# Kernel tuning notes

Hardware: AMD Instinct MI355X
Metric: run time of the kernel (lower is better)

The kernel has to match this reference:

```python
import jax, jax.numpy as jnp
import numpy as np

N = 8192      # number of graph nodes
C = 256       # feature_size
D = C // 2    # projection dim


def setup_inputs() -> dict:
    key = jax.random.key(0)
    ks = jax.random.split(key, 10)
    s_in = 1.0 / np.sqrt(C + 3)   # torch Linear default init scale (uniform bound)
    s_r = 1.0 / np.sqrt(D)
    return {
        "landmarks": jax.random.normal(ks[0], (1, N, 3), dtype=jnp.float32),
        "features": jax.random.normal(ks[1], (1, N, C), dtype=jnp.float32),
        # weights stored [in, out]
        "Wi": jax.random.uniform(ks[2], (C + 3, D), jnp.float32, -s_in, s_in),
        "bi": jax.random.uniform(ks[3], (D,), jnp.float32, -s_in, s_in),
        "Wj": jax.random.uniform(ks[4], (C + 3, D), jnp.float32, -s_in, s_in),
        "bj": jax.random.uniform(ks[5], (D,), jnp.float32, -s_in, s_in),
        "Wk": jax.random.uniform(ks[6], (C + 3, D), jnp.float32, -s_in, s_in),
        "bk": jax.random.uniform(ks[7], (D,), jnp.float32, -s_in, s_in),
        "Wr": jax.random.uniform(ks[8], (D, C), jnp.float32, -s_r, s_r),
        "br": jax.random.uniform(ks[9], (C,), jnp.float32, -s_r, s_r),
    }


def reference(landmarks, features, Wi, bi, Wj, bj, Wk, bk, Wr, br):
    # concat coords + features, drop the singleton batch dim: [N, C+3]
    x = jnp.concatenate([landmarks, features], axis=2)[0]
    fi = x @ Wi + bi                       # [N, D]
    fj = x @ Wj + bj                       # [N, D]
    fk = x @ Wk + bk                       # [N, D]
    att = jax.nn.sigmoid(fi @ fj.T)        # [N, N] sigmoid scores (non-softmax)
    att = att / jnp.sum(att, axis=1, keepdims=True)  # row-sum normalize
    out = (att @ fk) @ Wr + br             # [N, C] restored
    return features + out[None]            # residual, back to [1, N, C]
```

## Files before the change

kernel.cpp:

```cpp
#include <hip/hip_runtime.h>
#include <stdint.h>

#define N_NODES 8192
#define KPAD 272
#define OUTC 384

typedef __attribute__((ext_vector_type(8))) short bhalf8;
typedef __attribute__((ext_vector_type(16))) float f32x16;
typedef __attribute__((ext_vector_type(4))) float f32x4;

__device__ inline unsigned short f2bf_rne(float f) {
    unsigned u = __builtin_bit_cast(unsigned, f);
    u += 0x7FFFu + ((u >> 16) & 1u);
    return (unsigned short)(u >> 16);
}

__device__ inline bhalf8 mk8(unsigned a, unsigned b, unsigned c, unsigned d) {
    union { unsigned u[4]; bhalf8 v; } U;
    U.u[0] = a; U.u[1] = b; U.u[2] = c; U.u[3] = d;
    return U.v;
}

#define GLD_TO_LDS(gptr, lptr)                                                              \
    __builtin_amdgcn_global_load_lds((const __attribute__((address_space(1))) void*)(gptr), \
                                     (__attribute__((address_space(3))) void*)(lptr), 16, 0, 0)

__global__ void k_prep(const float* __restrict__ Wi, const float* __restrict__ bi,
                       const float* __restrict__ Wj, const float* __restrict__ bj,
                       const float* __restrict__ Wk, const float* __restrict__ bk,
                       const float* __restrict__ Wr,
                       unsigned short* __restrict__ WcatT, unsigned short* __restrict__ WrT,
                       float* __restrict__ bcat) {
    int idx = blockIdx.x * 256 + threadIdx.x;
    const int WC_N = OUTC * KPAD;
    const int WR_N = 256 * 128;
    if (idx < WC_N) {
        int n = idx / KPAD, kk = idx - n * KPAD;
        int sel = n >> 7, d = n & 127;
        const float* W = (sel == 0) ? Wi : ((sel == 1) ? Wj : Wk);
        float v = 0.f;
        if (kk < 256) v = W[(kk + 3) * 128 + d];
        else if (kk < 259) v = W[(kk - 256) * 128 + d];
        WcatT[idx] = f2bf_rne(v);
        return;
    }
    idx -= WC_N;
    if (idx < WR_N) {
        int c = idx >> 7, d = idx & 127;
        WrT[idx] = f2bf_rne(Wr[d * 256 + c]);
        return;
    }
    idx -= WR_N;
    if (idx < OUTC) {
        float v = (idx < 128) ? bi[idx] : ((idx < 256) ? bj[idx - 128] : bk[idx - 256]);
        bcat[idx] = v;
    }
}

__global__ __launch_bounds__(256) void k_proj(const float* __restrict__ landmarks,
                                              const float* __restrict__ features,
                                              const unsigned short* __restrict__ WcatT,
                                              const float* __restrict__ bcat,
                                              unsigned short* __restrict__ fi,
                                              unsigned short* __restrict__ fj,
                                              unsigned short* __restrict__ fkT) {
    const int tid = threadIdx.x, w = tid >> 6, l = tid & 63, h = l >> 5, ln = l & 31;
    const unsigned bid = blockIdx.x;
    const int it = bid / 3, ng = bid - it * 3;
    const int i0 = it * 32;
    const int n = ng * 128 + w * 32 + ln;
    const int row = i0 + ln;
    f32x16 acc = {};
#pragma unroll
    for (int s = 0; s < 17; ++s) {
        union { unsigned short us[8]; bhalf8 v; } A;
        if (s < 16) {
            const float* fp = features + (size_t)row * 256 + s * 16 + h * 8;
            f32x4 v0 = *(const f32x4*)(fp);
            f32x4 v1 = *(const f32x4*)(fp + 4);
#pragma unroll
            for (int e = 0; e < 4; ++e) { A.us[e] = f2bf_rne(v0[e]); A.us[4 + e] = f2bf_rne(v1[e]); }
        } else {
#pragma unroll
            for (int e = 0; e < 8; ++e) A.us[e] = 0;
            if (h == 0) {
                A.us[0] = f2bf_rne(landmarks[row * 3 + 0]);
                A.us[1] = f2bf_rne(landmarks[row * 3 + 1]);
                A.us[2] = f2bf_rne(landmarks[row * 3 + 2]);
            }
        }
        bhalf8 b = *(const bhalf8*)(WcatT + (size_t)n * KPAD + s * 16 + h * 8);
        acc = __builtin_amdgcn_mfma_f32_32x32x16_bf16(A.v, b, acc, 0, 0, 0);
    }
    const int d = w * 32 + ln;
    const float bias = bcat[n];
    if (ng < 2) {
        unsigned short* dst = ng ? fj : fi;
#pragma unroll
        for (int q = 0; q < 4; ++q) {
            int ib = i0 + 8 * q + 4 * h;
#pragma unroll
            for (int r = 0; r < 4; ++r)
                dst[(size_t)(ib + r) * 128 + d] = f2bf_rne(acc[4 * q + r] + bias);
        }
    } else {
#pragma unroll
        for (int q = 0; q < 4; ++q) {
            int ib = i0 + 8 * q + 4 * h;
            ushort4 pk;
            pk.x = f2bf_rne(acc[4 * q + 0] + bias);
            pk.y = f2bf_rne(acc[4 * q + 1] + bias);
            pk.z = f2bf_rne(acc[4 * q + 2] + bias);
            pk.w = f2bf_rne(acc[4 * q + 3] + bias);
            *(ushort4*)(fkT + (size_t)d * N_NODES + ib) = pk;
        }
    }
}

__global__ __launch_bounds__(256, 2) void k_attn(const unsigned short* __restrict__ fi,
                                                 const unsigned short* __restrict__ fj,
                                                 const unsigned short* __restrict__ fkT,
                                                 float* __restrict__ num_part,
                                                 float* __restrict__ den_part) {
    __shared__ __align__(16) char smem[65536];
    char* const fjb0 = smem;
    char* const fkb0 = smem + 16384;
    char* const fjb1 = smem + 32768;
    char* const fkb1 = smem + 49152;

    const int tid = threadIdx.x;
    const int w = tid >> 6, l = tid & 63, h = l >> 5, ln = l & 31;
    const int ih = w >> 1, jh = w & 1;
    const int rt = blockIdx.x & 127, jq = blockIdx.x >> 7;
    const int i0 = rt * 64;
    const int jbase = jq * 2048;

    const int rsub = l >> 4, cph = l & 15;

    bhalf8 bfi[8];
#pragma unroll
    for (int s = 0; s < 8; ++s)
        bfi[s] = *(const bhalf8*)(fi + (size_t)(i0 + ih * 32 + ln) * 128 + s * 16 + h * 8);

    f32x16 acc[4] = {};
    float dacc = 0.f;

    auto STAGE = [&](char* fjd, char* fkd, int J0) {
#pragma unroll
        for (int q = 0; q < 4; ++q) {
            int r = w * 16 + q * 4 + rsub;
            int c = cph ^ (r & 15);
            GLD_TO_LDS(fj + (size_t)(J0 + r) * 128 + c * 8, fjd + (w * 16 + q * 4) * 256);
        }
#pragma unroll
        for (int q = 0; q < 4; ++q) {
            int r = w * 16 + q * 4 + rsub;
            int g = cph ^ (r & 15);
            int d = r + ((g >> 3) << 6);
            int joff = (g & 7) * 8;
            GLD_TO_LDS(fkT + (size_t)d * N_NODES + J0 + joff, fkd + (w * 16 + q * 4) * 256);
        }
    };

    auto COMPUTE = [&](const char* fjbuf, const char* fkbuf) {
        f32x16 st = {};
        const int jrow = jh * 32 + ln;
        __builtin_amdgcn_s_setprio(1);
#pragma unroll
        for (int s = 0; s < 8; ++s) {
            int c = (s * 2 + h) ^ (jrow & 15);
            bhalf8 af = *(const bhalf8*)(fjbuf + jrow * 256 + c * 16);
            st = __builtin_amdgcn_mfma_f32_32x32x16_bf16(af, bfi[s], st, 0, 0, 0);
        }
        __builtin_amdgcn_s_setprio(0);
        unsigned p[8], xw[8];
#pragma unroll
        for (int q = 0; q < 8; ++q) {
            float x0 = __builtin_amdgcn_rcpf(1.f + __builtin_amdgcn_exp2f(st[2 * q] * -1.44269504f));
            float x1 = __builtin_amdgcn_rcpf(1.f + __builtin_amdgcn_exp2f(st[2 * q + 1] * -1.44269504f));
            dacc += x0;
            dacc += x1;
            p[q] = __builtin_amdgcn_perm(__builtin_bit_cast(unsigned, x1),
                                         __builtin_bit_cast(unsigned, x0), 0x07060302u);
        }
#pragma unroll
        for (int q = 0; q < 8; ++q) xw[q] = (unsigned)__shfl_xor((int)p[q], 32, 64);
        bhalf8 fb[2];
        if (h == 0) {
            fb[0] = mk8(p[0], p[1], xw[0], xw[1]);
            fb[1] = mk8(p[4], p[5], xw[4], xw[5]);
        } else {
            fb[0] = mk8(xw[2], xw[3], p[2], p[3]);
            fb[1] = mk8(xw[6], xw[7], p[6], p[7]);
        }
        __builtin_amdgcn_s_setprio(1);
#pragma unroll
        for (int m4 = 0; m4 < 4; ++m4) {
            int d = m4 * 32 + ln;
            int r = d & 63;
            int ghi = (d >> 6) << 3;
#pragma unroll
            for (int s2 = 0; s2 < 2; ++s2) {
                int g = ghi | (jh * 4 + s2 * 2 + h);
                int slot = g ^ (r & 15);
                bhalf8 af = *(const bhalf8*)(fkbuf + r * 256 + slot * 16);
                acc[m4] = __builtin_amdgcn_mfma_f32_32x32x16_bf16(af, fb[s2], acc[m4], 0, 0, 0);
            }
        }
        __builtin_amdgcn_s_setprio(0);
    };

    STAGE(fjb0, fkb0, jbase);
    __syncthreads();
#pragma unroll 1
    for (int mt = 0; mt < 32; mt += 2) {
        STAGE(fjb1, fkb1, jbase + (mt + 1) * 64);
        COMPUTE(fjb0, fkb0);
        __syncthreads();
        if (mt + 2 < 32) STAGE(fjb0, fkb0, jbase + (mt + 2) * 64);
        COMPUTE(fjb1, fkb1);
        __syncthreads();
    }

    dacc += __shfl_xor(dacc, 32, 64);
    float* denb = (float*)(smem + 40960);
    if (h == 0) denb[w * 32 + ln] = dacc;

    float* buf = (float*)smem;
    if (jh == 0) {
#pragma unroll
        for (int m4 = 0; m4 < 4; ++m4)
#pragma unroll
            for (int q = 0; q < 4; ++q) {
                f32x4 v = {acc[m4][4 * q + 0], acc[m4][4 * q + 1],
                           acc[m4][4 * q + 2], acc[m4][4 * q + 3]};
                *(f32x4*)(buf + (ih * 32 + ln) * 132 + m4 * 32 + 8 * q + 4 * h) = v;
            }
    }
    __syncthreads();
    if (jh == 1) {
#pragma unroll
        for (int m4 = 0; m4 < 4; ++m4)
#pragma unroll
            for (int q = 0; q < 4; ++q) {
                float* p4 = buf + (ih * 32 + ln) * 132 + m4 * 32 + 8 * q + 4 * h;
                f32x4 old = *(f32x4*)p4;
                f32x4 v = {acc[m4][4 * q + 0], acc[m4][4 * q + 1],
                           acc[m4][4 * q + 2], acc[m4][4 * q + 3]};
                *(f32x4*)p4 = old + v;
            }
    }
    __syncthreads();
#pragma unroll
    for (int e = 0; e < 8; ++e) {
        int v = e * 256 + tid;
        int iloc = v >> 5, d4 = (v & 31) * 4;
        *(f32x4*)(num_part + ((size_t)jq * N_NODES + i0 + iloc) * 128 + d4) =
            *(const f32x4*)(buf + iloc * 132 + d4);
    }
    if (tid < 64) {
        den_part[(size_t)jq * N_NODES + i0 + tid] =
            denb[(tid >> 5) * 64 + (tid & 31)] + denb[(tid >> 5) * 64 + 32 + (tid & 31)];
    }
}

__global__ __launch_bounds__(256) void k_out(const unsigned short* __restrict__ WrT,
                                             const float* __restrict__ br,
                                             const float* __restrict__ features,
                                             const float* __restrict__ num_part,
                                             const float* __restrict__ den_part,
                                             float* __restrict__ out) {
    __shared__ __align__(16) char smem[73728];
    char* const tb = smem + 65536;
    const int tid = threadIdx.x, w = tid >> 6, l = tid & 63, h = l >> 5, ln = l & 31;
    const int i0 = blockIdx.x * 32;
    {
        int rsub = l >> 4, cph = l & 15;
#pragma unroll
        for (int q = 0; q < 16; ++q) {
            int r = w * 64 + q * 4 + rsub;
            int c = cph ^ (r & 15);
            GLD_TO_LDS(WrT + (size_t)r * 128 + c * 8, smem + (w * 64 + q * 4) * 256);
        }
    }
    {
        int i = tid >> 3, dseg = (tid & 7) * 16;
        f32x4 s[4] = {};
        float ds = 0.f;
#pragma unroll
        for (int q = 0; q < 4; ++q) {
            const float* np = num_part + ((size_t)(q * N_NODES + i0 + i)) * 128 + dseg;
#pragma unroll
            for (int k = 0; k < 4; ++k) s[k] += *(const f32x4*)(np + 4 * k);
            ds += den_part[(size_t)q * N_NODES + i0 + i];
        }
        float inv = 1.0f / ds;
#pragma unroll
        for (int cc = 0; cc < 2; ++cc) {
            union { unsigned u[4]; bhalf8 v; } U;
#pragma unroll
            for (int m = 0; m < 4; ++m) {
                int e0 = cc * 8 + 2 * m;
                unsigned lo = f2bf_rne(s[e0 >> 2][e0 & 3] * inv);
                unsigned hi = f2bf_rne(s[(e0 + 1) >> 2][(e0 + 1) & 3] * inv);
                U.u[m] = lo | (hi << 16);
            }
            int slot = ((tid & 7) * 2 + cc) ^ (i & 15);
            *(bhalf8*)(tb + i * 256 + slot * 16) = U.v;
        }
    }
    __syncthreads();
    f32x16 acc[2] = {};
#pragma unroll
    for (int s = 0; s < 8; ++s) {
        int ca = (s * 2 + h) ^ (ln & 15);
        bhalf8 af = *(const bhalf8*)(tb + ln * 256 + ca * 16);
#pragma unroll
        for (int nt = 0; nt < 2; ++nt) {
            int row = w * 64 + nt * 32 + ln;
            int c = (s * 2 + h) ^ (row & 15);
            bhalf8 bf = *(const bhalf8*)(smem + row * 256 + c * 16);
            acc[nt] = __builtin_amdgcn_mfma_f32_32x32x16_bf16(af, bf, acc[nt], 0, 0, 0);
        }
    }
#pragma unroll
    for (int nt = 0; nt < 2; ++nt) {
        int cc = w * 64 + nt * 32 + ln;
        float bias = br[cc];
#pragma unroll
        for (int q = 0; q < 4; ++q) {
#pragma unroll
            for (int r = 0; r < 4; ++r) {
                int i = i0 + 8 * q + 4 * h + r;
                out[(size_t)i * 256 + cc] = acc[nt][4 * q + r] + bias + features[(size_t)i * 256 + cc];
            }
        }
    }
}

extern "C" void kernel_launch(void* const* d_in, const int* in_sizes, int n_in,
                              void* d_out, int out_size, void* d_ws, size_t ws_size,
                              hipStream_t stream) {
    const float* landmarks = (const float*)d_in[0];
    const float* features  = (const float*)d_in[1];
    const float* Wi = (const float*)d_in[2];
    const float* bi = (const float*)d_in[3];
    const float* Wj = (const float*)d_in[4];
    const float* bj = (const float*)d_in[5];
    const float* Wk = (const float*)d_in[6];
    const float* bk = (const float*)d_in[7];
    const float* Wr = (const float*)d_in[8];
    const float* br = (const float*)d_in[9];

    char* ws = (char*)d_ws;
    unsigned short* WcatT   = (unsigned short*)(ws + 0);
    unsigned short* WrT     = (unsigned short*)(ws + 208896);
    float*          bcat    = (float*)(ws + 274432);
    unsigned short* fi      = (unsigned short*)(ws + 275968);
    unsigned short* fjp     = (unsigned short*)(ws + 2373120);
    unsigned short* fkT     = (unsigned short*)(ws + 4470272);
    float*          num_part= (float*)(ws + 6567424);
    float*          den_part= (float*)(ws + 23344640);

    float* out = (float*)d_out;

    hipLaunchKernelGGL(k_prep, dim3(538), dim3(256), 0, stream,
                       Wi, bi, Wj, bj, Wk, bk, Wr, WcatT, WrT, bcat);
    hipLaunchKernelGGL(k_proj, dim3(768), dim3(256), 0, stream,
                       landmarks, features, WcatT, bcat, fi, fjp, fkT);
    hipLaunchKernelGGL(k_attn, dim3(512), dim3(256), 0, stream, fi, fjp, fkT, num_part, den_part);
    hipLaunchKernelGGL(k_out, dim3(256), dim3(256), 0, stream,
                       WrT, br, features, num_part, den_part, out);
}
```

Before: 151.6 us.

## Remap attention blocks per XCD, split MFMA chains, use permlane32 swap

Remaps the block index so that blocks on the same XCD (assuming round-robin dispatch over 8 XCDs) share the same key quarter and nearby row tiles, to improve L2 reuse of fj/fk. The score MFMA chain is split into two independent accumulators that are summed before the sigmoid, shortening the dependent MFMA chain. The shfl_xor-based exchange between half-waves is replaced with v_permlane32_swap, and the second PV MFMA group is split so it can start after the first swap. This adds one extra accumulator's worth of registers and an extra add per element, which may affect occupancy.

```diff
diff --git a/kernel.cpp b/kernel.cpp
--- a/kernel.cpp
+++ b/kernel.cpp
@@ -19,6 +19,10 @@
     union { unsigned u[4]; bhalf8 v; } U;
     U.u[0] = a; U.u[1] = b; U.u[2] = c; U.u[3] = d;
     return U.v;
+}
+
+__device__ inline void pl32swap(unsigned& a, unsigned& b) {
+    asm("v_permlane32_swap_b32 %0, %1" : "+v"(a), "+v"(b));
 }
 
 #define GLD_TO_LDS(gptr, lptr)                                                              \
@@ -131,7 +135,10 @@
     const int tid = threadIdx.x;
     const int w = tid >> 6, l = tid & 63, h = l >> 5, ln = l & 31;
     const int ih = w >> 1, jh = w & 1;
-    const int rt = blockIdx.x & 127, jq = blockIdx.x >> 7;
+    const unsigned b = blockIdx.x;
+    const int xcd = b & 7;
+    const int jq = xcd >> 1;
+    const int rt = (int)(b >> 3) + ((xcd & 1) << 6);
     const int i0 = rt * 64;
     const int jbase = jq * 2048;
 
@@ -163,49 +170,56 @@
     };
 
     auto COMPUTE = [&](const char* fjbuf, const char* fkbuf) {
-        f32x16 st = {};
+        f32x16 sa = {}, sb = {};
         const int jrow = jh * 32 + ln;
         __builtin_amdgcn_s_setprio(1);
 #pragma unroll
-        for (int s = 0; s < 8; ++s) {
-            int c = (s * 2 + h) ^ (jrow & 15);
-            bhalf8 af = *(const bhalf8*)(fjbuf + jrow * 256 + c * 16);
-            st = __builtin_amdgcn_mfma_f32_32x32x16_bf16(af, bfi[s], st, 0, 0, 0);
+        for (int ss = 0; ss < 4; ++ss) {
+            int se = 2 * ss, so = 2 * ss + 1;
+            int ce = (se * 2 + h) ^ (jrow & 15);
+            int co = (so * 2 + h) ^ (jrow & 15);
+            bhalf8 ae = *(const bhalf8*)(fjbuf + jrow * 256 + ce * 16);
+            bhalf8 ao = *(const bhalf8*)(fjbuf + jrow * 256 + co * 16);
+            sa = __builtin_amdgcn_mfma_f32_32x32x16_bf16(ae, bfi[se], sa, 0, 0, 0);
+            sb = __builtin_amdgcn_mfma_f32_32x32x16_bf16(ao, bfi[so], sb, 0, 0, 0);
         }
         __builtin_amdgcn_s_setprio(0);
-        unsigned p[8], xw[8];
+        unsigned p[8];
 #pragma unroll
         for (int q = 0; q < 8; ++q) {
-            float x0 = __builtin_amdgcn_rcpf(1.f + __builtin_amdgcn_exp2f(st[2 * q] * -1.44269504f));
-            float x1 = __builtin_amdgcn_rcpf(1.f + __builtin_amdgcn_exp2f(st[2 * q + 1] * -1.44269504f));
+            float e0 = sa[2 * q] + sb[2 * q];
+            float e1 = sa[2 * q + 1] + sb[2 * q + 1];
+            float x0 = __builtin_amdgcn_rcpf(1.f + __builtin_amdgcn_exp2f(e0 * -1.44269504f));
+            float x1 = __builtin_amdgcn_rcpf(1.f + __builtin_amdgcn_exp2f(e1 * -1.44269504f));
             dacc += x0;
             dacc += x1;
             p[q] = __builtin_amdgcn_perm(__builtin_bit_cast(unsigned, x1),
                                          __builtin_bit_cast(unsigned, x0), 0x07060302u);
         }
-#pragma unroll
-        for (int q = 0; q < 8; ++q) xw[q] = (unsigned)__shfl_xor((int)p[q], 32, 64);
-        bhalf8 fb[2];
-        if (h == 0) {
-            fb[0] = mk8(p[0], p[1], xw[0], xw[1]);
-            fb[1] = mk8(p[4], p[5], xw[4], xw[5]);
-        } else {
-            fb[0] = mk8(xw[2], xw[3], p[2], p[3]);
-            fb[1] = mk8(xw[6], xw[7], p[6], p[7]);
-        }
+        unsigned w0 = p[0], w2 = p[2]; pl32swap(w0, w2);
+        unsigned w1 = p[1], w3 = p[3]; pl32swap(w1, w3);
+        bhalf8 fb0 = mk8(w0, w1, w2, w3);
         __builtin_amdgcn_s_setprio(1);
 #pragma unroll
         for (int m4 = 0; m4 < 4; ++m4) {
             int d = m4 * 32 + ln;
             int r = d & 63;
-            int ghi = (d >> 6) << 3;
-#pragma unroll
-            for (int s2 = 0; s2 < 2; ++s2) {
-                int g = ghi | (jh * 4 + s2 * 2 + h);
-                int slot = g ^ (r & 15);
-                bhalf8 af = *(const bhalf8*)(fkbuf + r * 256 + slot * 16);
-                acc[m4] = __builtin_amdgcn_mfma_f32_32x32x16_bf16(af, fb[s2], acc[m4], 0, 0, 0);
-            }
+            int g = ((d >> 6) << 3) | (jh * 4 + h);
+            int slot = g ^ (r & 15);
+            bhalf8 af = *(const bhalf8*)(fkbuf + r * 256 + slot * 16);
+            acc[m4] = __builtin_amdgcn_mfma_f32_32x32x16_bf16(af, fb0, acc[m4], 0, 0, 0);
+        }
+        unsigned w4 = p[4], w6 = p[6]; pl32swap(w4, w6);
+        unsigned w5 = p[5], w7 = p[7]; pl32swap(w5, w7);
+        bhalf8 fb1 = mk8(w4, w5, w6, w7);
+#pragma unroll
+        for (int m4 = 0; m4 < 4; ++m4) {
+            int d = m4 * 32 + ln;
+            int r = d & 63;
+            int g = ((d >> 6) << 3) | (jh * 4 + 2 + h);
+            int slot = g ^ (r & 15);
+            bhalf8 af = *(const bhalf8*)(fkbuf + r * 256 + slot * 16);
+            acc[m4] = __builtin_amdgcn_mfma_f32_32x32x16_bf16(af, fb1, acc[m4], 0, 0, 0);
         }
         __builtin_amdgcn_s_setprio(0);
     };
@@ -280,7 +294,7 @@
         for (int q = 0; q < 16; ++q) {
             int r = w * 64 + q * 4 + rsub;
             int c = cph ^ (r & 15);
-            GLD_TO_LDS(WrT + (size_t)r * 128 + c * 8, smem + (w * 64 + q * 4) * 256);
+            GLD_TO_LDS(WrT + (size_t)r * 128 + c * 8, (char*)smem + (w * 64 + q * 4) * 256);
         }
     }
     {
```

Result: no change. 151.7 us (+0.0%).
